# Kernel optimization log

Hardware: AMD Instinct MI355X
Metric: run time of the kernel (lower is better)

The kernel has to match this reference:

```python
import jax, jax.numpy as jnp
import numpy as np

N_NODES = 100000
N_EDGES = 1000000
EMB = 64
HID = 64
N_CLASSES = 1
LEAKY_SLOPE = 0.01  # flax.linen.leaky_relu default


def setup_inputs() -> dict:
    key = jax.random.key(0)
    k1, k2, k3, k4, k5 = jax.random.split(key, 5)
    node_ids = jnp.arange(N_NODES, dtype=jnp.int32)
    senders = jax.random.randint(k1, (N_EDGES,), 0, N_NODES, dtype=jnp.int32)
    receivers = jax.random.randint(k2, (N_EDGES,), 0, N_NODES, dtype=jnp.int32)
    embed_table = jax.random.normal(k3, (N_NODES, EMB), dtype=jnp.float32) * 0.05
    W1 = jax.random.normal(k4, (EMB, HID), dtype=jnp.float32) * (1.0 / np.sqrt(EMB))
    W2 = jax.random.normal(k5, (HID, N_CLASSES), dtype=jnp.float32) * (1.0 / np.sqrt(HID))
    b2 = jnp.zeros((N_CLASSES,), dtype=jnp.float32)
    return {"node_ids": node_ids, "senders": senders, "receivers": receivers,
            "embed_table": embed_table, "W1": W1, "W2": W2, "b2": b2}


def gcn_aggregate(x, senders, receivers, n_nodes, symmetric):
    # Faithful to jraph.GraphConvolution: update_node_fn is applied BEFORE this.
    if symmetric:
        ones = jnp.ones_like(senders, dtype=x.dtype)
        send_deg = jax.ops.segment_sum(ones, senders, num_segments=n_nodes)
        recv_deg = jax.ops.segment_sum(ones, receivers, num_segments=n_nodes)
        x = x * jax.lax.rsqrt(jnp.maximum(send_deg, 1.0))[:, None]
        x = jax.ops.segment_sum(x[senders], receivers, num_segments=n_nodes)  # [N, d]
        x = x * jax.lax.rsqrt(jnp.maximum(recv_deg, 1.0))[:, None]
    else:
        x = jax.ops.segment_sum(x[senders], receivers, num_segments=n_nodes)
    return x


def reference(node_ids, senders, receivers, embed_table, W1, W2, b2):
    n = node_ids.shape[0]
    # GraphMapFeatures(embed_node_fn=nn.Embed(...))
    x = embed_table[node_ids]                      # [N, EMB]
    # GraphConvolution(Dense(hidden, use_bias=False), symmetric_normalization=True)
    x = x @ W1                                     # [N, HID]
    x = gcn_aggregate(x, senders, receivers, n, symmetric=True)
    x = jax.nn.leaky_relu(x, negative_slope=LEAKY_SLOPE)
    # GraphConvolution(Dense(classes), symmetric_normalization=False)
    x = x @ W2 + b2                                # [N, C]
    x = gcn_aggregate(x, senders, receivers, n, symmetric=False)
    return jax.nn.sigmoid(x)
```

## Files before the change

kernel.cpp:

```cpp
#include <hip/hip_runtime.h>
#include <hip/hip_bf16.h>

#define N_NODES 100000
#define N_EDGES 1000000
#define SCAN_B 256
#define N_BLOCKS_RS ((N_NODES + 255) / 256)
#define N_BLOCKS_A  ((N_NODES + 63) / 64)
#define H_BLOCKS 1024

#define CHUNKS 40
#define CHUNK_E 25000
#define HWORDS 25000


__device__ __forceinline__ unsigned f32_to_bf16(float v) {
    unsigned u = __float_as_uint(v);
    return (u + 0x7fffu + ((u >> 16) & 1u)) >> 16;
}

__global__ void k_hist8(const int4* __restrict__ s4,
                        const int4* __restrict__ r4,
                        unsigned* __restrict__ ghist_s8,
                        unsigned* __restrict__ ghist_r8,
                        unsigned char* __restrict__ rank8) {
    __shared__ unsigned lds[HWORDS];
    int b   = blockIdx.x;
    int isR = (b < CHUNKS);
    int c   = isR ? b : b - CHUNKS;
    int t   = threadIdx.x;

    for (int w = t; w < HWORDS; w += 1024) lds[w] = 0u;
    __syncthreads();

    int beg = c * (CHUNK_E / 4);
    int end = beg + CHUNK_E / 4;
    if (isR) {
        for (int q = beg + t; q < end; q += 1024) {
            int4 v = r4[q];
            int sh0 = (v.x & 3) * 8, sh1 = (v.y & 3) * 8;
            int sh2 = (v.z & 3) * 8, sh3 = (v.w & 3) * 8;
            unsigned o0 = atomicAdd(&lds[v.x >> 2], 1u << sh0);
            unsigned o1 = atomicAdd(&lds[v.y >> 2], 1u << sh1);
            unsigned o2 = atomicAdd(&lds[v.z >> 2], 1u << sh2);
            unsigned o3 = atomicAdd(&lds[v.w >> 2], 1u << sh3);
            uchar4 rk;
            rk.x = (unsigned char)((o0 >> sh0) & 0xffu);
            rk.y = (unsigned char)((o1 >> sh1) & 0xffu);
            rk.z = (unsigned char)((o2 >> sh2) & 0xffu);
            rk.w = (unsigned char)((o3 >> sh3) & 0xffu);
            *(uchar4*)(rank8 + 4 * (size_t)q) = rk;
        }
    } else {
        for (int q = beg + t; q < end; q += 1024) {
            int4 v = s4[q];
            atomicAdd(&lds[v.x >> 2], 1u << ((v.x & 3) * 8));
            atomicAdd(&lds[v.y >> 2], 1u << ((v.y & 3) * 8));
            atomicAdd(&lds[v.z >> 2], 1u << ((v.z & 3) * 8));
            atomicAdd(&lds[v.w >> 2], 1u << ((v.w & 3) * 8));
        }
    }
    __syncthreads();

    uint4* __restrict__ dst =
        (uint4*)((isR ? ghist_r8 : ghist_s8) + (size_t)c * HWORDS);
    const uint4* lsrc = (const uint4*)lds;
    for (int w = t; w < HWORDS / 4; w += 1024) dst[w] = lsrc[w];
}

__global__ void k_scanA(const unsigned char* __restrict__ gs8,
                        const unsigned char* __restrict__ gr8,
                        unsigned char* __restrict__ base8,
                        int* __restrict__ part,
                        float* __restrict__ rs,
                        int* __restrict__ blockSums) {
    __shared__ int s[64];
    int t = threadIdx.x;
    int g = t >> 2, sl = t & 3;
    int node = blockIdx.x * 64 + g;
    int total = 0;
    if (node < N_NODES) {
        unsigned ss = 0;
#pragma unroll
        for (int k = 0; k < 10; ++k)
            ss += gs8[(size_t)(sl * 10 + k) * N_NODES + node];
        ss += __shfl_xor(ss, 1, 64);
        ss += __shfl_xor(ss, 2, 64);
        if (sl == 0) rs[node] = rsqrtf(fmaxf((float)ss, 1.0f));

        unsigned rv[10];
        unsigned rsum = 0;
#pragma unroll
        for (int k = 0; k < 10; ++k) {
            rv[k] = gr8[(size_t)(sl * 10 + k) * N_NODES + node];
            rsum += rv[k];
        }
        unsigned x = rsum;
        unsigned u1 = __shfl_up(x, 1, 4); if (sl >= 1) x += u1;
        unsigned u2 = __shfl_up(x, 2, 4); if (sl >= 2) x += u2;
        unsigned run = x - rsum;
        total = (int)__shfl(x, 3, 4);
#pragma unroll
        for (int k = 0; k < 10; ++k) {
            base8[(size_t)(sl * 10 + k) * N_NODES + node] = (unsigned char)run;
            run += rv[k];
        }
    }
    if (sl == 0) s[g] = total;
    __syncthreads();
    if (t < 64) {
        int v = s[t];
        int acc = v;
#pragma unroll
        for (int off = 1; off < 64; off <<= 1) {
            int y = __shfl_up(acc, off, 64);
            if (t >= off) acc += y;
        }
        s[t] = acc - v;
        if (t == 63) blockSums[blockIdx.x] = acc;
    }
    __syncthreads();
    if (sl == 0 && node < N_NODES) part[node] = s[g];
}

__global__ void k_scanCD_h(const int* __restrict__ part,
                           const int* __restrict__ blockSums,
                           int* __restrict__ row_start,
                           const float* __restrict__ emb,
                           const float* __restrict__ rs,
                           const float* __restrict__ W1,
                           unsigned short* __restrict__ h16) {
    __shared__ int s[SCAN_B];
    __shared__ int gsum[4];
    int t = threadIdx.x;
    int b = blockIdx.x;

    if (b < N_BLOCKS_RS) {
        int acc = 0;
        for (int j = t; j < 4 * b; j += SCAN_B) acc += blockSums[j];
        s[t] = acc;
        __syncthreads();
        for (int off = SCAN_B / 2; off > 0; off >>= 1) {
            if (t < off) s[t] += s[t + off];
            __syncthreads();
        }
        int blockOff = s[0];
        if (t < 4)
            gsum[t] = (4 * b + t < N_BLOCKS_A) ? blockSums[4 * b + t] : 0;
        __syncthreads();

        int gi = t >> 6;
        int goff = blockOff;
        if (gi > 0) goff += gsum[0];
        if (gi > 1) goff += gsum[1];
        if (gi > 2) goff += gsum[2];
        int n = b * SCAN_B + t;
        if (n < N_NODES) row_start[n] = goff + part[n];
        if (b == 0 && t == 0) row_start[N_NODES] = N_EDGES;
    } else {
        int lane = t & 63;
        int wib  = t >> 6;
        int gw   = (b - N_BLOCKS_RS) * 4 + wib;
        const int nw = H_BLOCKS * 4;

        float w1c[64];
#pragma unroll
        for (int k = 0; k < 64; ++k) w1c[k] = W1[k * 64 + lane];

        for (int n = gw; n < N_NODES; n += nw) {
            float e = emb[(size_t)n * 64 + lane] * rs[n];
            float a0 = 0.f, a1 = 0.f, a2 = 0.f, a3 = 0.f;
            int ei = __float_as_int(e);
#pragma unroll
            for (int k = 0; k < 16; ++k) {
                a0 += __int_as_float(__builtin_amdgcn_readlane(ei, 4 * k + 0)) * w1c[4 * k + 0];
                a1 += __int_as_float(__builtin_amdgcn_readlane(ei, 4 * k + 1)) * w1c[4 * k + 1];
                a2 += __int_as_float(__builtin_amdgcn_readlane(ei, 4 * k + 2)) * w1c[4 * k + 2];
                a3 += __int_as_float(__builtin_amdgcn_readlane(ei, 4 * k + 3)) * w1c[4 * k + 3];
            }
            float a = (a0 + a1) + (a2 + a3);
            h16[(size_t)n * 64 + lane] = (unsigned short)f32_to_bf16(a);
        }
    }
}

__global__ void k_fill(const int4* __restrict__ s4,
                       const int4* __restrict__ r4,
                       const uchar4* __restrict__ rk4,
                       const unsigned char* __restrict__ base8,
                       const int* __restrict__ row_start,
                       int* __restrict__ col) {
    int i = blockIdx.x * blockDim.x + threadIdx.x;
    if (i >= N_EDGES / 4) return;
    int c = (4 * i) / CHUNK_E;
    const unsigned char* __restrict__ bs = base8 + (size_t)c * N_NODES;
    int4 s = s4[i];
    int4 r = r4[i];
    uchar4 rk = rk4[i];
    col[row_start[r.x] + bs[r.x] + rk.x] = s.x;
    col[row_start[r.y] + bs[r.y] + rk.y] = s.y;
    col[row_start[r.z] + bs[r.z] + rk.z] = s.z;
    col[row_start[r.w] + bs[r.w] + rk.w] = s.w;
}

__global__ void k_agg_post(const int* __restrict__ row_start,
                           const int* __restrict__ col,
                           const uint4* __restrict__ h128,
                           const float* __restrict__ W2,
                           const float* __restrict__ b2,
                           float* __restrict__ z) {
    int wid  = (blockIdx.x * blockDim.x + threadIdx.x) >> 6;
    int lane = threadIdx.x & 63;
    if (wid >= N_NODES) return;
    int eslot = lane >> 3;
    int fq    = lane & 7;

    int start = row_start[wid];
    int end   = row_start[wid + 1];
    int i0 = start + eslot;
    int i1 = i0 + 8;
    bool p0 = i0 < end, p1 = i1 < end;
    int c0 = p0 ? col[i0] : 0;
    int c1 = p1 ? col[i1] : 0;
    uint4 u0 = h128[(size_t)c0 * 8 + fq];
    uint4 u1 = h128[(size_t)c1 * 8 + fq];
    if (!p0) { u0.x = 0u; u0.y = 0u; u0.z = 0u; u0.w = 0u; }
    if (!p1) { u1.x = 0u; u1.y = 0u; u1.z = 0u; u1.w = 0u; }

    float a0, a1, a2, a3, a4, a5, a6, a7;
    a0 = __uint_as_float(u0.x << 16)        + __uint_as_float(u1.x << 16);
    a1 = __uint_as_float(u0.x & 0xffff0000u) + __uint_as_float(u1.x & 0xffff0000u);
    a2 = __uint_as_float(u0.y << 16)        + __uint_as_float(u1.y << 16);
    a3 = __uint_as_float(u0.y & 0xffff0000u) + __uint_as_float(u1.y & 0xffff0000u);
    a4 = __uint_as_float(u0.z << 16)        + __uint_as_float(u1.z << 16);
    a5 = __uint_as_float(u0.z & 0xffff0000u) + __uint_as_float(u1.z & 0xffff0000u);
    a6 = __uint_as_float(u0.w << 16)        + __uint_as_float(u1.w << 16);
    a7 = __uint_as_float(u0.w & 0xffff0000u) + __uint_as_float(u1.w & 0xffff0000u);

    for (int i = i1 + 8; i < end; i += 8) {
        int sx = col[i];
        uint4 u = h128[(size_t)sx * 8 + fq];
        a0 += __uint_as_float(u.x << 16);
        a1 += __uint_as_float(u.x & 0xffff0000u);
        a2 += __uint_as_float(u.y << 16);
        a3 += __uint_as_float(u.y & 0xffff0000u);
        a4 += __uint_as_float(u.z << 16);
        a5 += __uint_as_float(u.z & 0xffff0000u);
        a6 += __uint_as_float(u.w << 16);
        a7 += __uint_as_float(u.w & 0xffff0000u);
    }
#pragma unroll
    for (int off = 8; off < 64; off <<= 1) {
        a0 += __shfl_xor(a0, off, 64);
        a1 += __shfl_xor(a1, off, 64);
        a2 += __shfl_xor(a2, off, 64);
        a3 += __shfl_xor(a3, off, 64);
        a4 += __shfl_xor(a4, off, 64);
        a5 += __shfl_xor(a5, off, 64);
        a6 += __shfl_xor(a6, off, 64);
        a7 += __shfl_xor(a7, off, 64);
    }
    float rsq = rsqrtf(fmaxf((float)(end - start), 1.0f));
    float4 wA = ((const float4*)W2)[fq * 2];
    float4 wB = ((const float4*)W2)[fq * 2 + 1];
    float p = 0.f, x;
    x = a0 * rsq; x = (x > 0.f) ? x : 0.01f * x; p += x * wA.x;
    x = a1 * rsq; x = (x > 0.f) ? x : 0.01f * x; p += x * wA.y;
    x = a2 * rsq; x = (x > 0.f) ? x : 0.01f * x; p += x * wA.z;
    x = a3 * rsq; x = (x > 0.f) ? x : 0.01f * x; p += x * wA.w;
    x = a4 * rsq; x = (x > 0.f) ? x : 0.01f * x; p += x * wB.x;
    x = a5 * rsq; x = (x > 0.f) ? x : 0.01f * x; p += x * wB.y;
    x = a6 * rsq; x = (x > 0.f) ? x : 0.01f * x; p += x * wB.z;
    x = a7 * rsq; x = (x > 0.f) ? x : 0.01f * x; p += x * wB.w;
    p += __shfl_xor(p, 1, 64);
    p += __shfl_xor(p, 2, 64);
    p += __shfl_xor(p, 4, 64);
    if (lane == 0) z[wid] = p + b2[0];
}

__global__ void k_agg2_sigmoid(const int* __restrict__ row_start,
                               const int* __restrict__ col,
                               const float* __restrict__ z,
                               float* __restrict__ out) {
    int gtid = blockIdx.x * blockDim.x + threadIdx.x;
    int n  = gtid >> 3;
    int sl = gtid & 7;
    if (n >= N_NODES) return;
    int start = row_start[n];
    int end   = row_start[n + 1];
    int i0 = start + sl;
    int i1 = i0 + 8;
    bool p0 = i0 < end, p1 = i1 < end;
    int c0 = p0 ? col[i0] : 0;
    int c1 = p1 ? col[i1] : 0;
    float z0 = z[c0];
    float z1 = z[c1];
    float acc = (p0 ? z0 : 0.f) + (p1 ? z1 : 0.f);
    for (int i = i1 + 8; i < end; i += 8) acc += z[col[i]];
    acc += __shfl_xor(acc, 1, 64);
    acc += __shfl_xor(acc, 2, 64);
    acc += __shfl_xor(acc, 4, 64);
    if (sl == 0) out[n] = 1.0f / (1.0f + expf(-acc));
}

extern "C" void kernel_launch(void* const* d_in, const int* in_sizes, int n_in,
                              void* d_out, int out_size, void* d_ws, size_t ws_size,
                              hipStream_t stream) {
    const int* senders    = (const int*)d_in[1];
    const int* receivers  = (const int*)d_in[2];
    const float* emb      = (const float*)d_in[3];
    const float* W1       = (const float*)d_in[4];
    const float* W2       = (const float*)d_in[5];
    const float* b2       = (const float*)d_in[6];
    float* out            = (float*)d_out;

    char* ws = (char*)d_ws;
    unsigned char*  ghist_s8  = (unsigned char*)(ws);
    unsigned char*  ghist_r8  = (unsigned char*)(ws + 4000000);
    unsigned char*  base8     = (unsigned char*)(ws + 8000000);
    unsigned char*  rank8     = (unsigned char*)(ws + 12000000);
    int*            part      = (int*)(ws + 13000000);
    int*            row_start = (int*)(ws + 13400000);
    int*            blockSums = (int*)(ws + 13800016);
    float*          rs        = (float*)(ws + 13807600);
    int*            col       = (int*)(ws + 14207600);
    unsigned short* h16       = (unsigned short*)(ws + 18207616);
    float*          z         = (float*)(ws + 31007616);

    const int B = 256;
    const int QBLK = (N_EDGES / 4 + B - 1) / B;

    k_hist8<<<2 * CHUNKS, 1024, 0, stream>>>(
        (const int4*)senders, (const int4*)receivers,
        (unsigned*)ghist_s8, (unsigned*)ghist_r8, rank8);
    k_scanA<<<N_BLOCKS_A, B, 0, stream>>>(
        ghist_s8, ghist_r8, base8, part, rs, blockSums);
    k_scanCD_h<<<N_BLOCKS_RS + H_BLOCKS, B, 0, stream>>>(
        part, blockSums, row_start, emb, rs, W1, h16);
    k_fill<<<QBLK, B, 0, stream>>>(
        (const int4*)senders, (const int4*)receivers,
        (const uchar4*)rank8, base8, row_start, col);
    k_agg_post<<<(N_NODES * 64) / B, B, 0, stream>>>(
        row_start, col, (const uint4*)h16, W2, b2, z);
    k_agg2_sigmoid<<<(N_NODES * 8 + B - 1) / B, B, 0, stream>>>(
        row_start, col, z, out);
}
```

Baseline: 183.0 us.

## Use split-bf16 MFMA for embedding matmul and double histogram chunk count

Replaces the per-node readlane FMA loop for the embedding x W1 product with 16-row tiles computed by bf16 MFMA instructions. Each fp32 operand is split into hi and lo bf16 parts to keep near-fp32 accuracy, at the cost of six MFMAs per output tile plus conversion work. Separately, the edge histogram uses twice as many chunks of half the size, so the hist kernel gets more blocks. This doubles the per-chunk histogram workspace and the scan work per node, and the workspace offsets are shifted to fit.

```diff
diff --git a/kernel.cpp b/kernel.cpp
--- a/kernel.cpp
+++ b/kernel.cpp
@@ -6,16 +6,24 @@
 #define SCAN_B 256
 #define N_BLOCKS_RS ((N_NODES + 255) / 256)
 #define N_BLOCKS_A  ((N_NODES + 63) / 64)
-#define H_BLOCKS 1024
-
-#define CHUNKS 40
-#define CHUNK_E 25000
+#define MLP_TILES (N_NODES / 16)
+#define MLP_BLOCKS 1563
+
+#define CHUNKS 80
+#define CHUNK_E 12500
 #define HWORDS 25000
-
+#define CPL 20
+
+
+typedef __attribute__((ext_vector_type(8))) short bf16x8;
+typedef __attribute__((ext_vector_type(4))) float f32x4;
 
 __device__ __forceinline__ unsigned f32_to_bf16(float v) {
     unsigned u = __float_as_uint(v);
     return (u + 0x7fffu + ((u >> 16) & 1u)) >> 16;
+}
+__device__ __forceinline__ float bf16_to_f32(unsigned h) {
+    return __uint_as_float(h << 16);
 }
 
 __global__ void k_hist8(const int4* __restrict__ s4,
@@ -81,17 +89,17 @@
     if (node < N_NODES) {
         unsigned ss = 0;
 #pragma unroll
-        for (int k = 0; k < 10; ++k)
-            ss += gs8[(size_t)(sl * 10 + k) * N_NODES + node];
+        for (int k = 0; k < CPL; ++k)
+            ss += gs8[(size_t)(sl * CPL + k) * N_NODES + node];
         ss += __shfl_xor(ss, 1, 64);
         ss += __shfl_xor(ss, 2, 64);
         if (sl == 0) rs[node] = rsqrtf(fmaxf((float)ss, 1.0f));
 
-        unsigned rv[10];
+        unsigned rv[CPL];
         unsigned rsum = 0;
 #pragma unroll
-        for (int k = 0; k < 10; ++k) {
-            rv[k] = gr8[(size_t)(sl * 10 + k) * N_NODES + node];
+        for (int k = 0; k < CPL; ++k) {
+            rv[k] = gr8[(size_t)(sl * CPL + k) * N_NODES + node];
             rsum += rv[k];
         }
         unsigned x = rsum;
@@ -100,8 +108,8 @@
         unsigned run = x - rsum;
         total = (int)__shfl(x, 3, 4);
 #pragma unroll
-        for (int k = 0; k < 10; ++k) {
-            base8[(size_t)(sl * 10 + k) * N_NODES + node] = (unsigned char)run;
+        for (int k = 0; k < CPL; ++k) {
+            base8[(size_t)(sl * CPL + k) * N_NODES + node] = (unsigned char)run;
             run += rv[k];
         }
     }
@@ -122,7 +130,7 @@
     if (sl == 0 && node < N_NODES) part[node] = s[g];
 }
 
-__global__ void k_scanCD_h(const int* __restrict__ part,
+__global__ void k_rows_mlp(const int* __restrict__ part,
                            const int* __restrict__ blockSums,
                            int* __restrict__ row_start,
                            const float* __restrict__ emb,
@@ -157,29 +165,62 @@
         if (n < N_NODES) row_start[n] = goff + part[n];
         if (b == 0 && t == 0) row_start[N_NODES] = N_EDGES;
     } else {
+        int wg = (b - N_BLOCKS_RS) * 4 + (t >> 6);
+        if (wg >= MLP_TILES) return;
         int lane = t & 63;
-        int wib  = t >> 6;
-        int gw   = (b - N_BLOCKS_RS) * 4 + wib;
-        const int nw = H_BLOCKS * 4;
-
-        float w1c[64];
-#pragma unroll
-        for (int k = 0; k < 64; ++k) w1c[k] = W1[k * 64 + lane];
-
-        for (int n = gw; n < N_NODES; n += nw) {
-            float e = emb[(size_t)n * 64 + lane] * rs[n];
-            float a0 = 0.f, a1 = 0.f, a2 = 0.f, a3 = 0.f;
-            int ei = __float_as_int(e);
-#pragma unroll
-            for (int k = 0; k < 16; ++k) {
-                a0 += __int_as_float(__builtin_amdgcn_readlane(ei, 4 * k + 0)) * w1c[4 * k + 0];
-                a1 += __int_as_float(__builtin_amdgcn_readlane(ei, 4 * k + 1)) * w1c[4 * k + 1];
-                a2 += __int_as_float(__builtin_amdgcn_readlane(ei, 4 * k + 2)) * w1c[4 * k + 2];
-                a3 += __int_as_float(__builtin_amdgcn_readlane(ei, 4 * k + 3)) * w1c[4 * k + 3];
+        int r  = lane & 15;
+        int kh = lane >> 4;
+        int n0 = wg * 16;
+        int nrow = n0 + r;
+
+        float rsv = rs[nrow];
+        const float* __restrict__ erow = emb + (size_t)nrow * 64 + 8 * kh;
+
+        bf16x8 ehiA, eloA, ehiB, eloB;
+#pragma unroll
+        for (int j = 0; j < 8; ++j) {
+            float xa = erow[j] * rsv;
+            unsigned ha = f32_to_bf16(xa);
+            ehiA[j] = (short)ha;
+            eloA[j] = (short)f32_to_bf16(xa - bf16_to_f32(ha));
+            float xb = erow[32 + j] * rsv;
+            unsigned hb = f32_to_bf16(xb);
+            ehiB[j] = (short)hb;
+            eloB[j] = (short)f32_to_bf16(xb - bf16_to_f32(hb));
+        }
+
+        bf16x8 whi[4][2], wlo[4][2];
+#pragma unroll
+        for (int nt = 0; nt < 4; ++nt)
+#pragma unroll
+            for (int h2 = 0; h2 < 2; ++h2)
+#pragma unroll
+                for (int j = 0; j < 8; ++j) {
+                    float w = W1[(size_t)(h2 * 32 + 8 * kh + j) * 64 + nt * 16 + r];
+                    unsigned hw = f32_to_bf16(w);
+                    whi[nt][h2][j] = (short)hw;
+                    wlo[nt][h2][j] = (short)f32_to_bf16(w - bf16_to_f32(hw));
+                }
+
+        f32x4 acc[4];
+#pragma unroll
+        for (int nt = 0; nt < 4; ++nt) {
+            acc[nt] = (f32x4)0.f;
+            acc[nt] = __builtin_amdgcn_mfma_f32_16x16x32_bf16(ehiA, wlo[nt][0], acc[nt], 0, 0, 0);
+            acc[nt] = __builtin_amdgcn_mfma_f32_16x16x32_bf16(eloA, whi[nt][0], acc[nt], 0, 0, 0);
+            acc[nt] = __builtin_amdgcn_mfma_f32_16x16x32_bf16(ehiB, wlo[nt][1], acc[nt], 0, 0, 0);
+            acc[nt] = __builtin_amdgcn_mfma_f32_16x16x32_bf16(eloB, whi[nt][1], acc[nt], 0, 0, 0);
+            acc[nt] = __builtin_amdgcn_mfma_f32_16x16x32_bf16(ehiA, whi[nt][0], acc[nt], 0, 0, 0);
+            acc[nt] = __builtin_amdgcn_mfma_f32_16x16x32_bf16(ehiB, whi[nt][1], acc[nt], 0, 0, 0);
+        }
+#pragma unroll
+        for (int nt = 0; nt < 4; ++nt)
+#pragma unroll
+            for (int j = 0; j < 4; ++j) {
+                int row = kh * 4 + j;
+                h16[(size_t)(n0 + row) * 64 + nt * 16 + r] =
+                    (unsigned short)f32_to_bf16(acc[nt][j]);
             }
-            float a = (a0 + a1) + (a2 + a3);
-            h16[(size_t)n * 64 + lane] = (unsigned short)f32_to_bf16(a);
-        }
     }
 }
 
@@ -315,16 +356,16 @@
 
     char* ws = (char*)d_ws;
     unsigned char*  ghist_s8  = (unsigned char*)(ws);
-    unsigned char*  ghist_r8  = (unsigned char*)(ws + 4000000);
-    unsigned char*  base8     = (unsigned char*)(ws + 8000000);
-    unsigned char*  rank8     = (unsigned char*)(ws + 12000000);
-    int*            part      = (int*)(ws + 13000000);
-    int*            row_start = (int*)(ws + 13400000);
-    int*            blockSums = (int*)(ws + 13800016);
-    float*          rs        = (float*)(ws + 13807600);
-    int*            col       = (int*)(ws + 14207600);
-    unsigned short* h16       = (unsigned short*)(ws + 18207616);
-    float*          z         = (float*)(ws + 31007616);
+    unsigned char*  ghist_r8  = (unsigned char*)(ws + 8000000);
+    unsigned char*  base8     = (unsigned char*)(ws + 16000000);
+    unsigned char*  rank8     = (unsigned char*)(ws + 24000000);
+    int*            part      = (int*)(ws + 25000000);
+    int*            row_start = (int*)(ws + 25400000);
+    int*            blockSums = (int*)(ws + 25800016);
+    float*          rs        = (float*)(ws + 25806272);
+    int*            col       = (int*)(ws + 26206272);
+    unsigned short* h16       = (unsigned short*)(ws + 30206336);
+    float*          z         = (float*)(ws + 43006336);
 
     const int B = 256;
     const int QBLK = (N_EDGES / 4 + B - 1) / B;
@@ -334,7 +375,7 @@
         (unsigned*)ghist_s8, (unsigned*)ghist_r8, rank8);
     k_scanA<<<N_BLOCKS_A, B, 0, stream>>>(
         ghist_s8, ghist_r8, base8, part, rs, blockSums);
-    k_scanCD_h<<<N_BLOCKS_RS + H_BLOCKS, B, 0, stream>>>(
+    k_rows_mlp<<<N_BLOCKS_RS + MLP_BLOCKS, B, 0, stream>>>(
         part, blockSums, row_start, emb, rs, W1, h16);
     k_fill<<<QBLK, B, 0, stream>>>(
         (const int4*)senders, (const int4*)receivers,
```

New measurement: 179.0 us (median of 2 runs). 2.2% less time.
